# Optimization experiments

Measured on AMD Instinct MI355X. Metric: run time of the kernel, lower is better.

Reference implementation:

```python
import jax, jax.numpy as jnp
import numpy as np

B, S, DM, H = 4, 1024, 1024, 16
DK = DM // H  # 64, must equal embeddim=64

def _linear(x, W, b):
    # torch nn.Linear: y = x @ W.T + b, W is [out, in]
    return jnp.matmul(x, W.T) + b

def setup_inputs() -> dict:
    key = jax.random.key(0)
    ks = jax.random.split(key, 40)
    inp = {}
    inp["query"] = jax.random.normal(ks[0], (B, S, DM), jnp.float32)
    inp["key"] = jax.random.normal(ks[1], (B, S, DM), jnp.float32)
    inp["value"] = jax.random.normal(ks[2], (B, S, DM), jnp.float32)
    inp["mask"] = jnp.ones((B, S, S), jnp.int32)
    def mk(i, dout, din):
        W = jax.random.normal(ks[i], (dout, din), jnp.float32) / np.sqrt(din).astype(np.float32)
        b = jax.random.normal(ks[i + 20], (dout,), jnp.float32) * 0.01
        return W, b
    # the 4 d_model x d_model projection linears (q, k, v, out)
    inp["Wq"], inp["bq"] = mk(3, DM, DM)
    inp["Wk"], inp["bk"] = mk(4, DM, DM)
    inp["Wv"], inp["bv"] = mk(5, DM, DM)
    inp["Wo"], inp["bo"] = mk(6, DM, DM)
    # the 64x64 refinement linears
    inp["Wkl"], inp["bkl"] = mk(7, DK, DK)   # key_linear
    inp["Wql"], inp["bql"] = mk(8, DK, DK)   # query_linear
    inp["Wq2"], inp["bq2"] = mk(9, DK, DK)   # query2_linear
    inp["Wvl"], inp["bvl"] = mk(10, DK, DK)  # value_linear
    inp["Wel"], inp["bel"] = mk(11, DK, DK)  # embed_linear
    return inp

def reference(query, key, value, mask,
              Wq, bq, Wk, bk, Wv, bv, Wo, bo,
              Wkl, bkl, Wql, bql, Wq2, bq2, Wvl, bvl, Wel, bel):
    b, s, dm = query.shape
    # project and split heads: [b, h, s, d_k]
    def split(x):
        return x.reshape(b, s, H, DK).transpose(0, 2, 1, 3)
    q = split(_linear(query, Wq, bq))
    k = split(_linear(key, Wk, bk))
    v = split(_linear(value, Wv, bv))
    # per-head 64x64 refinements with relu
    key_refine = jax.nn.relu(_linear(k, Wkl, bkl))
    q1 = jax.nn.relu(_linear(q, Wql, bql))
    q1 = jax.nn.relu(_linear(q1, Wel, bel))
    q2 = jax.nn.relu(_linear(q, Wq2, bq2))
    v_refine = jax.nn.relu(_linear(v, Wvl, bvl))
    # two attention-like matmuls (no 1/sqrt(d_k) scaling in original)
    qv = jnp.einsum("bhqd,bhkd->bhqk", q2, v_refine)
    kq = jnp.einsum("bhqd,bhkd->bhqk", q1, key_refine)
    m = mask[:, None, :, :]  # mask.unsqueeze(1)
    kq = jnp.where(m == 0, jnp.float32(-1e9), kq)
    attn = jax.nn.softmax(kq, axis=-1)
    # elementwise combine, then matmul against raw projected key (not value!)
    out = jnp.einsum("bhqk,bhkd->bhqd", attn * qv, k)
    out = out.transpose(0, 2, 1, 3).reshape(b, s, dm)
    return _linear(out, Wo, bo)
```

## Files before the change

kernel.cpp:

```cpp
#include <hip/hip_runtime.h>
#include <hip/hip_bf16.h>

#define B_  4
#define S_  1024
#define DM_ 1024
#define H_  16
#define DK_ 64

typedef unsigned short u16;
typedef __attribute__((ext_vector_type(8))) short bf16x8;
typedef __attribute__((ext_vector_type(4))) float f32x4;

__device__ __forceinline__ float bf2f(u16 u) {
    union { unsigned int i; float f; } c;
    c.i = ((unsigned int)u) << 16;
    return c.f;
}
__device__ __forceinline__ u16 f2bf(float f) {
    union { float f; unsigned int i; } c;
    c.f = f;
    unsigned int x = c.i;
    unsigned int lsb = (x >> 16) & 1u;
    x += 0x7fffu + lsb;
    return (u16)(x >> 16);
}
__device__ __forceinline__ u16 f2bf_fast(float f) {
    __hip_bfloat16 h = __float2bfloat16(f);
    return *reinterpret_cast<u16*>(&h);
}

__device__ __forceinline__ void async_ld16(const u16* g, u16* l) {
    __builtin_amdgcn_global_load_lds(
        (const __attribute__((address_space(1))) unsigned int*)(const void*)g,
        (__attribute__((address_space(3))) unsigned int*)(void*)l, 16, 0, 0);
}

__global__ void detect_kernel(const u16* __restrict__ q, int* __restrict__ flag) {
    int lane = threadIdx.x & 63;
    int cnt = 0;
#pragma unroll
    for (int i = 0; i < 4; ++i) {
        u16 u = q[2 * (lane * 4 + i)];
        int e = (u >> 7) & 0xFF;
        cnt += (e >= 100 && e <= 140) ? 1 : 0;
    }
#pragma unroll
    for (int off = 1; off < 64; off <<= 1) cnt += __shfl_xor(cnt, off, 64);
    if (lane == 0) *flag = (cnt < 128) ? 1 : 0;
}

#define NSEG 12
struct CvtArgs {
    const void* src[NSEG];
    void*       dst[NSEG];
    unsigned    off[NSEG + 1];
};

__global__ __launch_bounds__(256) void prep_kernel(
    CvtArgs a, unsigned total, const int* __restrict__ flag,
    const int* __restrict__ mask, int* __restrict__ tflags)
{
    const int tid = threadIdx.x;
    if (blockIdx.x < 512) {
        const int bx = blockIdx.x;
        const int kt = bx & 15, b = (bx >> 4) & 3, z = bx >> 6;
        int ok = 1;
#pragma unroll
        for (int i = tid; i < 128 * 16; i += 256) {
            int row = z * 128 + (i >> 4), seg = i & 15;
            int4 m = *(const int4*)&mask[((size_t)b * S_ + row) * S_ + kt * 64 + seg * 4];
            ok &= (m.x != 0) & (m.y != 0) & (m.z != 0) & (m.w != 0);
        }
        if (!ok) atomicOr(&tflags[b * 16 + kt], 1);
        return;
    }
    if (!*flag) return;
    unsigned v = (blockIdx.x - 512) * 256 + tid;
    if (v >= total) return;
    int s = 0;
    while (s < NSEG - 1 && v >= a.off[s + 1]) ++s;
    unsigned local = v - a.off[s];
    u16* dp = (u16*)a.dst[s] + (size_t)local * 8;
    const float* sp = (const float*)a.src[s] + (size_t)local * 8;
    float4 x = *(const float4*)sp, y = *(const float4*)(sp + 4);
    u16 t[8] = {f2bf(x.x), f2bf(x.y), f2bf(x.z), f2bf(x.w),
                f2bf(y.x), f2bf(y.y), f2bf(y.z), f2bf(y.w)};
    *(uint4*)dp = *(uint4*)t;
}

__global__ __launch_bounds__(256) void transpose_kernel(
    const u16* __restrict__ kp, u16* __restrict__ kpt)
{
    __shared__ u16 T[64][65];
    const int s0 = blockIdx.x * 64, h = blockIdx.y, b = blockIdx.z;
    const int tid = threadIdx.x;
    const size_t base = (size_t)b * S_ * DM_ + (size_t)h * DK_;
    for (int c = tid; c < 512; c += 256) {
        int row = c >> 3, cc = (c & 7) * 8;
        union { uint4 v; u16 u[8]; } x;
        x.v = *(const uint4*)&kp[base + (size_t)(s0 + row) * DM_ + cc];
#pragma unroll
        for (int j = 0; j < 8; ++j) T[row][cc + j] = x.u[j];
    }
    __syncthreads();
    const size_t baseT = (size_t)(b * H_ + h) * DK_ * S_;
    for (int c = tid; c < 512; c += 256) {
        int d = c >> 3, ss = (c & 7) * 8;
        u16 t[8];
#pragma unroll
        for (int j = 0; j < 8; ++j) t[j] = T[ss + j][d];
        *(uint4*)&kpt[baseT + (size_t)d * S_ + s0 + ss] = *(uint4*)t;
    }
}

struct QKVArgs {
    const u16* A0[3]; const u16* A1[3];
    const u16* W0[3]; const u16* W1[3];
    const void* bias[3];
    const u16* R10[3]; const u16* R11[3];
    const void* rb1[3];
    const u16* R20; const u16* R21; const void* rb2;
    const u16* R30; const u16* R31; const void* rb3;
    u16 *Kp, *q1b, *q2r, *krb, *vrb;
};

__global__ __launch_bounds__(256, 3) void qkv_fused_kernel(
    QKVArgs a, const int* __restrict__ flag)
{
    __shared__ __align__(16) u16 smem[16384];
    u16 (*As)[64] = (u16(*)[64])smem;
    u16 (*Ws)[64] = (u16(*)[64])(smem + 8192);

    const int z = blockIdx.z;
    const int f = *flag;
    const u16* __restrict__ A = f ? a.A1[z] : a.A0[z];
    const u16* __restrict__ W = f ? a.W1[z] : a.W0[z];
    const void* biasp = a.bias[z];

    const int m0   = blockIdx.y * 128;
    const int n0   = blockIdx.x * 128;
    const int tid  = threadIdx.x;
    const int w    = tid >> 6;
    const int lane = tid & 63;
    const int l16  = lane & 15;
    const int quad = lane >> 4;
    const int wr   = (w >> 1) * 64;
    const int wc   = (w & 1) * 64;

    const int srow = lane >> 3;
    const int sgrp = (lane & 7) ^ srow;

    f32x4 acc[4][4];
#pragma unroll
    for (int rt = 0; rt < 4; ++rt)
#pragma unroll
        for (int ct = 0; ct < 4; ++ct) acc[rt][ct] = (f32x4){0.f, 0.f, 0.f, 0.f};

    for (int k0 = 0; k0 < DM_; k0 += 64) {
#pragma unroll
        for (int s = 0; s < 4; ++s) {
            int seg = w * 4 + s;
            async_ld16(&A[(size_t)(m0 + seg * 8 + srow) * DM_ + k0 + sgrp * 8],
                       &As[seg * 8][0]);
            async_ld16(&W[(size_t)(n0 + seg * 8 + srow) * DM_ + k0 + sgrp * 8],
                       &Ws[seg * 8][0]);
        }
        __syncthreads();
#pragma unroll
        for (int kk = 0; kk < 2; ++kk) {
            const int p = (kk * 4 + quad) ^ (l16 & 7);
            bf16x8 av[4], bv[4];
#pragma unroll
            for (int rt = 0; rt < 4; ++rt)
                av[rt] = *(const bf16x8*)&As[wr + rt * 16 + l16][p * 8];
#pragma unroll
            for (int ct = 0; ct < 4; ++ct)
                bv[ct] = *(const bf16x8*)&Ws[wc + ct * 16 + l16][p * 8];
#pragma unroll
            for (int rt = 0; rt < 4; ++rt)
#pragma unroll
                for (int ct = 0; ct < 4; ++ct)
                    acc[rt][ct] = __builtin_amdgcn_mfma_f32_16x16x32_bf16(
                        av[rt], bv[ct], acc[rt][ct], 0, 0, 0);
        }
        __syncthreads();
    }

    const int hcol = n0 + wc;
    u16 (*Es)[64] = (u16(*)[64])(smem + w * 4096);

#pragma unroll
    for (int ct = 0; ct < 4; ++ct) {
        int col = hcol + ct * 16 + l16;
        float bv = f ? ((const float*)biasp)[col] : bf2f(((const u16*)biasp)[col]);
#pragma unroll
        for (int rt = 0; rt < 4; ++rt)
#pragma unroll
            for (int r = 0; r < 4; ++r) {
                int ml = rt * 16 + quad * 4 + r;
                int cl = ct * 16 + l16;
                u16 bb = f2bf(acc[rt][ct][r] + bv);
                if (z == 1) a.Kp[(size_t)(m0 + wr + ml) * DM_ + col] = bb;
                Es[ml][((((cl >> 3) ^ (ml & 7)) << 3) | (cl & 7))] = bb;
            }
    }

    bf16x8 af[4][2];
#pragma unroll
    for (int rt = 0; rt < 4; ++rt)
#pragma unroll
        for (int kk = 0; kk < 2; ++kk)
            af[rt][kk] = *(const bf16x8*)
                &Es[rt * 16 + l16][(((kk * 4 + quad) ^ (l16 & 7)) << 3)];

    const u16* R1 = f ? a.R11[z] : a.R10[z];
    bf16x8 wb[2][4];
#pragma unroll
    for (int kk = 0; kk < 2; ++kk)
#pragma unroll
        for (int ct = 0; ct < 4; ++ct)
            wb[kk][ct] = *(const bf16x8*)
                &R1[(size_t)(ct * 16 + l16) * 64 + kk * 32 + quad * 8];

    f32x4 r1[4][4];
#pragma unroll
    for (int rt = 0; rt < 4; ++rt)
#pragma unroll
        for (int ct = 0; ct < 4; ++ct) r1[rt][ct] = (f32x4){0.f, 0.f, 0.f, 0.f};
#pragma unroll
    for (int kk = 0; kk < 2; ++kk)
#pragma unroll
        for (int rt = 0; rt < 4; ++rt)
#pragma unroll
            for (int ct = 0; ct < 4; ++ct)
                r1[rt][ct] = __builtin_amdgcn_mfma_f32_16x16x32_bf16(
                    af[rt][kk], wb[kk][ct], r1[rt][ct], 0, 0, 0);

    if (z != 0) {
        const void* rb = a.rb1[z];
        u16* out = (z == 1) ? a.krb : a.vrb;
#pragma unroll
        for (int ct = 0; ct < 4; ++ct) {
            int cl = ct * 16 + l16;
            float bv = f ? ((const float*)rb)[cl] : bf2f(((const u16*)rb)[cl]);
#pragma unroll
            for (int rt = 0; rt < 4; ++rt)
#pragma unroll
                for (int r = 0; r < 4; ++r) {
                    float v = r1[rt][ct][r] + bv;
                    v = v > 0.f ? v : 0.f;
                    out[(size_t)(m0 + wr + rt * 16 + quad * 4 + r) * DM_ + hcol + cl]
                        = f2bf(v);
                }
        }
    } else {
        {
            const void* rb = a.rb1[0];
#pragma unroll
            for (int ct = 0; ct < 4; ++ct) {
                int cl = ct * 16 + l16;
                float bv = f ? ((const float*)rb)[cl] : bf2f(((const u16*)rb)[cl]);
#pragma unroll
                for (int rt = 0; rt < 4; ++rt)
#pragma unroll
                    for (int r = 0; r < 4; ++r) {
                        float v = r1[rt][ct][r] + bv;
                        v = v > 0.f ? v : 0.f;
                        int ml = rt * 16 + quad * 4 + r;
                        Es[ml][((((cl >> 3) ^ (ml & 7)) << 3) | (cl & 7))] = f2bf(v);
                    }
            }
        }
        {
            const u16* R3 = f ? a.R31 : a.R30;
#pragma unroll
            for (int kk = 0; kk < 2; ++kk)
#pragma unroll
                for (int ct = 0; ct < 4; ++ct)
                    wb[kk][ct] = *(const bf16x8*)
                        &R3[(size_t)(ct * 16 + l16) * 64 + kk * 32 + quad * 8];
            f32x4 r3[4][4];
#pragma unroll
            for (int rt = 0; rt < 4; ++rt)
#pragma unroll
                for (int ct = 0; ct < 4; ++ct) r3[rt][ct] = (f32x4){0.f, 0.f, 0.f, 0.f};
#pragma unroll
            for (int kk = 0; kk < 2; ++kk)
#pragma unroll
                for (int rt = 0; rt < 4; ++rt)
#pragma unroll
                    for (int ct = 0; ct < 4; ++ct)
                        r3[rt][ct] = __builtin_amdgcn_mfma_f32_16x16x32_bf16(
                            af[rt][kk], wb[kk][ct], r3[rt][ct], 0, 0, 0);
            const void* rb = a.rb3;
#pragma unroll
            for (int ct = 0; ct < 4; ++ct) {
                int cl = ct * 16 + l16;
                float bv = f ? ((const float*)rb)[cl] : bf2f(((const u16*)rb)[cl]);
#pragma unroll
                for (int rt = 0; rt < 4; ++rt)
#pragma unroll
                    for (int r = 0; r < 4; ++r) {
                        float v = r3[rt][ct][r] + bv;
                        v = v > 0.f ? v : 0.f;
                        a.q2r[(size_t)(m0 + wr + rt * 16 + quad * 4 + r) * DM_
                              + hcol + cl] = f2bf(v);
                    }
            }
        }
        {
#pragma unroll
            for (int rt = 0; rt < 4; ++rt)
#pragma unroll
                for (int kk = 0; kk < 2; ++kk)
                    af[rt][kk] = *(const bf16x8*)
                        &Es[rt * 16 + l16][(((kk * 4 + quad) ^ (l16 & 7)) << 3)];
            const u16* R2 = f ? a.R21 : a.R20;
#pragma unroll
            for (int kk = 0; kk < 2; ++kk)
#pragma unroll
                for (int ct = 0; ct < 4; ++ct)
                    wb[kk][ct] = *(const bf16x8*)
                        &R2[(size_t)(ct * 16 + l16) * 64 + kk * 32 + quad * 8];
            f32x4 r2[4][4];
#pragma unroll
            for (int rt = 0; rt < 4; ++rt)
#pragma unroll
                for (int ct = 0; ct < 4; ++ct) r2[rt][ct] = (f32x4){0.f, 0.f, 0.f, 0.f};
#pragma unroll
            for (int kk = 0; kk < 2; ++kk)
#pragma unroll
                for (int rt = 0; rt < 4; ++rt)
#pragma unroll
                    for (int ct = 0; ct < 4; ++ct)
                        r2[rt][ct] = __builtin_amdgcn_mfma_f32_16x16x32_bf16(
                            af[rt][kk], wb[kk][ct], r2[rt][ct], 0, 0, 0);
            const void* rb = a.rb2;
#pragma unroll
            for (int ct = 0; ct < 4; ++ct) {
                int cl = ct * 16 + l16;
                float bv = f ? ((const float*)rb)[cl] : bf2f(((const u16*)rb)[cl]);
#pragma unroll
                for (int rt = 0; rt < 4; ++rt)
#pragma unroll
                    for (int r = 0; r < 4; ++r) {
                        float v = r2[rt][ct][r] + bv;
                        v = v > 0.f ? v : 0.f;
                        a.q1b[(size_t)(m0 + wr + rt * 16 + quad * 4 + r) * DM_
                              + hcol + cl] = f2bf(v);
                    }
            }
        }
    }
}

__global__ __launch_bounds__(256, 3) void gemm_async_kernel(
    const u16* __restrict__ Ain, const u16* __restrict__ W0,
    const u16* __restrict__ W1, const void* __restrict__ biasp,
    void* __restrict__ Cp, const int* __restrict__ flag)
{
    __shared__ __align__(16) u16 As[128][64];
    __shared__ __align__(16) u16 Ws[128][64];

    const int f = *flag;
    const u16* __restrict__ W = f ? W1 : W0;

    const int m0   = blockIdx.y * 128;
    const int n0   = blockIdx.x * 128;
    const int tid  = threadIdx.x;
    const int w    = tid >> 6;
    const int lane = tid & 63;
    const int l16  = lane & 15;
    const int quad = lane >> 4;
    const int wr   = (w >> 1) * 64;
    const int wc   = (w & 1) * 64;

    const int srow = lane >> 3;
    const int sgrp = (lane & 7) ^ srow;

    f32x4 acc[4][4];
#pragma unroll
    for (int rt = 0; rt < 4; ++rt)
#pragma unroll
        for (int ct = 0; ct < 4; ++ct) acc[rt][ct] = (f32x4){0.f, 0.f, 0.f, 0.f};

    for (int k0 = 0; k0 < DM_; k0 += 64) {
#pragma unroll
        for (int s = 0; s < 4; ++s) {
            int seg = w * 4 + s;
            async_ld16(&Ain[(size_t)(m0 + seg * 8 + srow) * DM_ + k0 + sgrp * 8],
                       &As[seg * 8][0]);
            async_ld16(&W[(size_t)(n0 + seg * 8 + srow) * DM_ + k0 + sgrp * 8],
                       &Ws[seg * 8][0]);
        }
        __syncthreads();
#pragma unroll
        for (int kk = 0; kk < 2; ++kk) {
            const int p = (kk * 4 + quad) ^ (l16 & 7);
            bf16x8 av[4], bv[4];
#pragma unroll
            for (int rt = 0; rt < 4; ++rt)
                av[rt] = *(const bf16x8*)&As[wr + rt * 16 + l16][p * 8];
#pragma unroll
            for (int ct = 0; ct < 4; ++ct)
                bv[ct] = *(const bf16x8*)&Ws[wc + ct * 16 + l16][p * 8];
#pragma unroll
            for (int rt = 0; rt < 4; ++rt)
#pragma unroll
                for (int ct = 0; ct < 4; ++ct)
                    acc[rt][ct] = __builtin_amdgcn_mfma_f32_16x16x32_bf16(
                        av[rt], bv[ct], acc[rt][ct], 0, 0, 0);
        }
        __syncthreads();
    }

#pragma unroll
    for (int ct = 0; ct < 4; ++ct) {
        int col = n0 + wc + ct * 16 + l16;
        float bv = f ? ((const float*)biasp)[col] : bf2f(((const u16*)biasp)[col]);
#pragma unroll
        for (int rt = 0; rt < 4; ++rt)
#pragma unroll
            for (int r = 0; r < 4; ++r) {
                int row = m0 + wr + rt * 16 + quad * 4 + r;
                float v = acc[rt][ct][r] + bv;
                size_t idx = (size_t)row * DM_ + col;
                if (f) ((float*)Cp)[idx] = v;
                else   ((u16*)Cp)[idx]   = f2bf(v);
            }
    }
}

__global__ __launch_bounds__(256, 2) void attn_kernel(
    const u16* __restrict__ q1, const u16* __restrict__ q2,
    const u16* __restrict__ kr, const u16* __restrict__ vr,
    const u16* __restrict__ kpt, const int* __restrict__ mask,
    const int* __restrict__ tflags, u16* __restrict__ om)
{
    __shared__ __align__(16) u16 krs[64][72];
    __shared__ __align__(16) u16 vrs[64][72];
    __shared__ __align__(16) u16 kts[64][72];
    __shared__ __align__(16) u16 pts[4][32][72];

    const int qt   = blockIdx.x;
    const int h    = blockIdx.y;
    const int b    = blockIdx.z;
    const int q0   = qt * 128;
    const int tid  = threadIdx.x;
    const int w    = tid >> 6;
    const int lane = tid & 63;
    const int l16  = lane & 15;
    const int quad = lane >> 4;

    const size_t base  = (size_t)b * S_ * DM_ + (size_t)h * DK_;
    const size_t baseT = (size_t)(b * H_ + h) * DK_ * S_;

    bf16x8 a1[2][2], a2[2][2];
#pragma unroll
    for (int rt = 0; rt < 2; ++rt) {
        const int qrow = q0 + w * 32 + rt * 16 + l16;
#pragma unroll
        for (int kk = 0; kk < 2; ++kk) {
            a1[rt][kk] = *(const bf16x8*)&q1[base + (size_t)qrow * DM_ + kk * 32 + quad * 8];
            a2[rt][kk] = *(const bf16x8*)&q2[base + (size_t)qrow * DM_ + kk * 32 + quad * 8];
        }
    }

    float m_run[2][4], l_run[2][4];
    f32x4 oacc[2][4];
#pragma unroll
    for (int rt = 0; rt < 2; ++rt)
#pragma unroll
        for (int r = 0; r < 4; ++r) { m_run[rt][r] = -1e30f; l_run[rt][r] = 0.f; }
#pragma unroll
    for (int rt = 0; rt < 2; ++rt)
#pragma unroll
        for (int ct = 0; ct < 4; ++ct) oacc[rt][ct] = (f32x4){0.f, 0.f, 0.f, 0.f};

    for (int kt = 0; kt < S_ / 64; ++kt) {
        const int k0 = kt * 64;
        __syncthreads();
        for (int c = tid; c < 512; c += 256) {
            int row = c >> 3, cc = (c & 7) * 8;
            *(uint4*)&krs[row][cc] = *(const uint4*)&kr[base + (size_t)(k0 + row) * DM_ + cc];
            *(uint4*)&vrs[row][cc] = *(const uint4*)&vr[base + (size_t)(k0 + row) * DM_ + cc];
            *(uint4*)&kts[row][cc] = *(const uint4*)&kpt[baseT + (size_t)row * S_ + k0 + cc];
        }
        __syncthreads();

        const int tf = tflags[b * 16 + kt];

        f32x4 s1[2][4], s2[2][4];
#pragma unroll
        for (int rt = 0; rt < 2; ++rt)
#pragma unroll
            for (int ct = 0; ct < 4; ++ct) {
                s1[rt][ct] = (f32x4){0.f, 0.f, 0.f, 0.f};
                s2[rt][ct] = (f32x4){0.f, 0.f, 0.f, 0.f};
            }
#pragma unroll
        for (int kk = 0; kk < 2; ++kk) {
            bf16x8 b1[4], b2[4];
#pragma unroll
            for (int ct = 0; ct < 4; ++ct) {
                b1[ct] = *(const bf16x8*)&krs[ct * 16 + l16][kk * 32 + quad * 8];
                b2[ct] = *(const bf16x8*)&vrs[ct * 16 + l16][kk * 32 + quad * 8];
            }
#pragma unroll
            for (int rt = 0; rt < 2; ++rt)
#pragma unroll
                for (int ct = 0; ct < 4; ++ct) {
                    s1[rt][ct] = __builtin_amdgcn_mfma_f32_16x16x32_bf16(
                        a1[rt][kk], b1[ct], s1[rt][ct], 0, 0, 0);
                    s2[rt][ct] = __builtin_amdgcn_mfma_f32_16x16x32_bf16(
                        a2[rt][kk], b2[ct], s2[rt][ct], 0, 0, 0);
                }
        }

        if (tf) {
#pragma unroll
            for (int rt = 0; rt < 2; ++rt)
#pragma unroll
                for (int ct = 0; ct < 4; ++ct)
#pragma unroll
                    for (int r = 0; r < 4; ++r) {
                        int qrow = q0 + w * 32 + rt * 16 + quad * 4 + r;
                        int kc   = k0 + ct * 16 + l16;
                        if (mask[((size_t)b * S_ + qrow) * S_ + kc] == 0)
                            s1[rt][ct][r] = -1e9f;
                    }
        }

        float tmax[2][4];
#pragma unroll
        for (int rt = 0; rt < 2; ++rt)
#pragma unroll
            for (int r = 0; r < 4; ++r) tmax[rt][r] = -1e30f;
#pragma unroll
        for (int rt = 0; rt < 2; ++rt)
#pragma unroll
            for (int ct = 0; ct < 4; ++ct)
#pragma unroll
                for (int r = 0; r < 4; ++r)
                    tmax[rt][r] = fmaxf(tmax[rt][r], s1[rt][ct][r]);
#pragma unroll
        for (int off = 1; off < 16; off <<= 1)
#pragma unroll
            for (int rt = 0; rt < 2; ++rt)
#pragma unroll
                for (int r = 0; r < 4; ++r)
                    tmax[rt][r] = fmaxf(tmax[rt][r], __shfl_xor(tmax[rt][r], off, 64));

        float alpha[2][4], newm[2][4];
#pragma unroll
        for (int rt = 0; rt < 2; ++rt)
#pragma unroll
            for (int r = 0; r < 4; ++r) {
                newm[rt][r]  = fmaxf(m_run[rt][r], tmax[rt][r]);
                alpha[rt][r] = __expf(m_run[rt][r] - newm[rt][r]);
                m_run[rt][r] = newm[rt][r];
            }

        float psum[2][4] = {};
#pragma unroll
        for (int rt = 0; rt < 2; ++rt)
#pragma unroll
            for (int ct = 0; ct < 4; ++ct)
#pragma unroll
                for (int r = 0; r < 4; ++r) {
                    float p = __expf(s1[rt][ct][r] - newm[rt][r]);
                    psum[rt][r] += p;
                    pts[w][rt * 16 + quad * 4 + r][ct * 16 + l16] =
                        f2bf_fast(p * s2[rt][ct][r]);
                }
#pragma unroll
        for (int off = 1; off < 16; off <<= 1)
#pragma unroll
            for (int rt = 0; rt < 2; ++rt)
#pragma unroll
                for (int r = 0; r < 4; ++r)
                    psum[rt][r] += __shfl_xor(psum[rt][r], off, 64);
#pragma unroll
        for (int rt = 0; rt < 2; ++rt)
#pragma unroll
            for (int r = 0; r < 4; ++r)
                l_run[rt][r] = l_run[rt][r] * alpha[rt][r] + psum[rt][r];
#pragma unroll
        for (int rt = 0; rt < 2; ++rt)
#pragma unroll
            for (int ct = 0; ct < 4; ++ct)
#pragma unroll
                for (int r = 0; r < 4; ++r) oacc[rt][ct][r] *= alpha[rt][r];

        {
            bf16x8 bb[2][4];
#pragma unroll
            for (int kk = 0; kk < 2; ++kk)
#pragma unroll
                for (int ct = 0; ct < 4; ++ct)
                    bb[kk][ct] = *(const bf16x8*)&kts[ct * 16 + l16][kk * 32 + quad * 8];
#pragma unroll
            for (int rt = 0; rt < 2; ++rt)
#pragma unroll
                for (int kk = 0; kk < 2; ++kk) {
                    bf16x8 a = *(const bf16x8*)&pts[w][rt * 16 + l16][kk * 32 + quad * 8];
#pragma unroll
                    for (int ct = 0; ct < 4; ++ct)
                        oacc[rt][ct] = __builtin_amdgcn_mfma_f32_16x16x32_bf16(
                            a, bb[kk][ct], oacc[rt][ct], 0, 0, 0);
                }
        }
    }

#pragma unroll
    for (int rt = 0; rt < 2; ++rt)
#pragma unroll
        for (int ct = 0; ct < 4; ++ct)
#pragma unroll
            for (int r = 0; r < 4; ++r) {
                int row = q0 + w * 32 + rt * 16 + quad * 4 + r;
                int col = ct * 16 + l16;
                float v = oacc[rt][ct][r] / l_run[rt][r];
                om[base + (size_t)row * DM_ + col] = f2bf_fast(v);
            }
}

extern "C" void kernel_launch(void* const* d_in, const int* in_sizes, int n_in,
                              void* d_out, int out_size, void* d_ws, size_t ws_size,
                              hipStream_t stream)
{
    const void* query = d_in[0];
    const void* key   = d_in[1];
    const void* value = d_in[2];
    const int*  mask  = (const int*)d_in[3];
    const void* Wq  = d_in[4];  const void* bq  = d_in[5];
    const void* Wk  = d_in[6];  const void* bk  = d_in[7];
    const void* Wv  = d_in[8];  const void* bv  = d_in[9];
    const void* Wo  = d_in[10]; const void* bo  = d_in[11];
    const void* Wkl = d_in[12]; const void* bkl = d_in[13];
    const void* Wql = d_in[14]; const void* bql = d_in[15];
    const void* Wq2 = d_in[16]; const void* bq2 = d_in[17];
    const void* Wvl = d_in[18]; const void* bvl = d_in[19];
    const void* Wel = d_in[20]; const void* bel = d_in[21];

    int* flag   = (int*)d_ws;
    int* tflags = (int*)d_ws + 4;
    u16* ws     = (u16*)((char*)d_ws + 512);
    const size_t BUF = (size_t)(B_ * S_) * DM_;
    u16* Kp  = ws + 0 * BUF;
    u16* krb = ws + 1 * BUF;
    u16* q1b = ws + 2 * BUF;
    u16* q2r = ws + 3 * BUF;
    u16* vrb = ws + 4 * BUF;
    u16* Om  = ws + 5 * BUF;
    u16* KpT = ws + 6 * BUF;
    u16* Qc  = ws + 7 * BUF;
    u16* Kc  = ws + 8 * BUF;
    u16* Vc  = ws + 9 * BUF;
    u16* Wbig = ws + 10 * BUF;
    u16* Wqc = Wbig + 0 * (size_t)(DM_ * DM_);
    u16* Wkc = Wbig + 1 * (size_t)(DM_ * DM_);
    u16* Wvc = Wbig + 2 * (size_t)(DM_ * DM_);
    u16* Woc = Wbig + 3 * (size_t)(DM_ * DM_);
    u16* Wsm = Wbig + 4 * (size_t)(DM_ * DM_);
    u16* Wklc = Wsm + 0 * (DK_ * DK_);
    u16* Wqlc = Wsm + 1 * (DK_ * DK_);
    u16* Welc = Wsm + 2 * (DK_ * DK_);
    u16* Wq2c = Wsm + 3 * (DK_ * DK_);
    u16* Wvlc = Wsm + 4 * (DK_ * DK_);

    const int M = B_ * S_;
    dim3 blk(256);

    detect_kernel<<<1, 64, 0, stream>>>((const u16*)query, flag);

    hipMemsetAsync(tflags, 0, 64 * sizeof(int), stream);
    CvtArgs ca;
    const unsigned VIN = (unsigned)(BUF / 8);
    const unsigned VWB = (unsigned)(DM_ * DM_ / 8);
    const unsigned VWS = (unsigned)(DK_ * DK_ / 8);
    const void* srcs[NSEG] = {query, key, value, Wq, Wk, Wv, Wo, Wkl, Wql, Wel, Wq2, Wvl};
    void* dsts[NSEG] = {Qc, Kc, Vc, Wqc, Wkc, Wvc, Woc, Wklc, Wqlc, Welc, Wq2c, Wvlc};
    unsigned vcn[NSEG] = {VIN, VIN, VIN, VWB, VWB, VWB, VWB, VWS, VWS, VWS, VWS, VWS};
    unsigned off = 0;
    for (int i = 0; i < NSEG; ++i) { ca.src[i] = srcs[i]; ca.dst[i] = dsts[i]; ca.off[i] = off; off += vcn[i]; }
    ca.off[NSEG] = off;
    prep_kernel<<<dim3(512 + (off + 255) / 256), blk, 0, stream>>>(ca, off, flag, mask, tflags);

    QKVArgs qa = {};
    qa.A0[0] = (const u16*)query; qa.A1[0] = Qc;
    qa.A0[1] = (const u16*)key;   qa.A1[1] = Kc;
    qa.A0[2] = (const u16*)value; qa.A1[2] = Vc;
    qa.W0[0] = (const u16*)Wq; qa.W1[0] = Wqc;
    qa.W0[1] = (const u16*)Wk; qa.W1[1] = Wkc;
    qa.W0[2] = (const u16*)Wv; qa.W1[2] = Wvc;
    qa.bias[0] = bq; qa.bias[1] = bk; qa.bias[2] = bv;
    qa.R10[0] = (const u16*)Wql; qa.R11[0] = Wqlc; qa.rb1[0] = bql;
    qa.R10[1] = (const u16*)Wkl; qa.R11[1] = Wklc; qa.rb1[1] = bkl;
    qa.R10[2] = (const u16*)Wvl; qa.R11[2] = Wvlc; qa.rb1[2] = bvl;
    qa.R20 = (const u16*)Wel; qa.R21 = Welc; qa.rb2 = bel;
    qa.R30 = (const u16*)Wq2; qa.R31 = Wq2c; qa.rb3 = bq2;
    qa.Kp = Kp; qa.q1b = q1b; qa.q2r = q2r; qa.krb = krb; qa.vrb = vrb;
    dim3 gBig(DM_ / 128, M / 128, 3);
    qkv_fused_kernel<<<gBig, blk, 0, stream>>>(qa, flag);

    dim3 gT(S_ / 64, H_, B_);
    transpose_kernel<<<gT, blk, 0, stream>>>(Kp, KpT);

    dim3 gA(S_ / 128, H_, B_);
    attn_kernel<<<gA, blk, 0, stream>>>(q1b, q2r, krb, vrb, KpT, mask, tflags, Om);

    dim3 gO(DM_ / 128, M / 128);
    gemm_async_kernel<<<gO, blk, 0, stream>>>(Om, (const u16*)Wo, Woc, bo, d_out, flag);
}
```

Baseline: 315.8 us.

## Double-buffer attention K/V tiles, swizzle blocks across XCDs, raise MFMA priority

The attention kernel now loads the next 64-key tile of key-refine, value-refine and transposed K into registers while the current tile is computed. It writes them into a second LDS buffer afterwards, so each iteration needs one barrier instead of two and global load latency is hidden. The 3D grid is flattened and remapped so consecutive blocks on the same XCD work on the same batch and head, aiming for better L2 reuse of K/V. s_setprio is raised around the MFMA sections. The cost is double the LDS for the K/V tiles, which may lower occupancy, plus extra registers for the prefetched data.

```diff
diff --git a/kernel.cpp b/kernel.cpp
--- a/kernel.cpp
+++ b/kernel.cpp
@@ -437,14 +437,17 @@
     const u16* __restrict__ kpt, const int* __restrict__ mask,
     const int* __restrict__ tflags, u16* __restrict__ om)
 {
-    __shared__ __align__(16) u16 krs[64][72];
-    __shared__ __align__(16) u16 vrs[64][72];
-    __shared__ __align__(16) u16 kts[64][72];
+    __shared__ __align__(16) u16 krs[2][64][72];
+    __shared__ __align__(16) u16 vrs[2][64][72];
+    __shared__ __align__(16) u16 kts[2][64][72];
     __shared__ __align__(16) u16 pts[4][32][72];
 
-    const int qt   = blockIdx.x;
-    const int h    = blockIdx.y;
-    const int b    = blockIdx.z;
+    const int bid  = blockIdx.x;
+    const int orig = (bid & 7) * 64 + (bid >> 3);
+    const int qt = orig & 7;
+    const int h  = (orig >> 3) & 15;
+    const int b  = orig >> 7;
+
     const int q0   = qt * 128;
     const int tid  = threadIdx.x;
     const int w    = tid >> 6;
@@ -455,6 +458,9 @@
     const size_t base  = (size_t)b * S_ * DM_ + (size_t)h * DK_;
     const size_t baseT = (size_t)(b * H_ + h) * DK_ * S_;
 
+    const int sr = tid >> 3;
+    const int sc = (tid & 7) * 8;
+
     bf16x8 a1[2][2], a2[2][2];
 #pragma unroll
     for (int rt = 0; rt < 2; ++rt) {
@@ -477,16 +483,37 @@
 #pragma unroll
         for (int ct = 0; ct < 4; ++ct) oacc[rt][ct] = (f32x4){0.f, 0.f, 0.f, 0.f};
 
+    {
+        uint4 ka = *(const uint4*)&kr[base + (size_t)(sr) * DM_ + sc];
+        uint4 kb = *(const uint4*)&kr[base + (size_t)(sr + 32) * DM_ + sc];
+        uint4 va = *(const uint4*)&vr[base + (size_t)(sr) * DM_ + sc];
+        uint4 vb = *(const uint4*)&vr[base + (size_t)(sr + 32) * DM_ + sc];
+        uint4 ta = *(const uint4*)&kpt[baseT + (size_t)sr * S_ + sc];
+        uint4 tb = *(const uint4*)&kpt[baseT + (size_t)(sr + 32) * S_ + sc];
+        *(uint4*)&krs[0][sr][sc]      = ka;
+        *(uint4*)&krs[0][sr + 32][sc] = kb;
+        *(uint4*)&vrs[0][sr][sc]      = va;
+        *(uint4*)&vrs[0][sr + 32][sc] = vb;
+        *(uint4*)&kts[0][sr][sc]      = ta;
+        *(uint4*)&kts[0][sr + 32][sc] = tb;
+    }
+    __syncthreads();
+
     for (int kt = 0; kt < S_ / 64; ++kt) {
-        const int k0 = kt * 64;
-        __syncthreads();
-        for (int c = tid; c < 512; c += 256) {
-            int row = c >> 3, cc = (c & 7) * 8;
-            *(uint4*)&krs[row][cc] = *(const uint4*)&kr[base + (size_t)(k0 + row) * DM_ + cc];
-            *(uint4*)&vrs[row][cc] = *(const uint4*)&vr[base + (size_t)(k0 + row) * DM_ + cc];
-            *(uint4*)&kts[row][cc] = *(const uint4*)&kpt[baseT + (size_t)row * S_ + k0 + cc];
-        }
-        __syncthreads();
+        const int cur = kt & 1;
+        const int k0  = kt * 64;
+        const bool pf = (kt + 1 < S_ / 64);
+
+        uint4 ka, kb, va, vb, ta, tb;
+        if (pf) {
+            const int kn = k0 + 64;
+            ka = *(const uint4*)&kr[base + (size_t)(kn + sr) * DM_ + sc];
+            kb = *(const uint4*)&kr[base + (size_t)(kn + sr + 32) * DM_ + sc];
+            va = *(const uint4*)&vr[base + (size_t)(kn + sr) * DM_ + sc];
+            vb = *(const uint4*)&vr[base + (size_t)(kn + sr + 32) * DM_ + sc];
+            ta = *(const uint4*)&kpt[baseT + (size_t)sr * S_ + kn + sc];
+            tb = *(const uint4*)&kpt[baseT + (size_t)(sr + 32) * S_ + kn + sc];
+        }
 
         const int tf = tflags[b * 16 + kt];
 
@@ -498,13 +525,14 @@
                 s1[rt][ct] = (f32x4){0.f, 0.f, 0.f, 0.f};
                 s2[rt][ct] = (f32x4){0.f, 0.f, 0.f, 0.f};
             }
+        __builtin_amdgcn_s_setprio(1);
 #pragma unroll
         for (int kk = 0; kk < 2; ++kk) {
             bf16x8 b1[4], b2[4];
 #pragma unroll
             for (int ct = 0; ct < 4; ++ct) {
-                b1[ct] = *(const bf16x8*)&krs[ct * 16 + l16][kk * 32 + quad * 8];
-                b2[ct] = *(const bf16x8*)&vrs[ct * 16 + l16][kk * 32 + quad * 8];
+                b1[ct] = *(const bf16x8*)&krs[cur][ct * 16 + l16][kk * 32 + quad * 8];
+                b2[ct] = *(const bf16x8*)&vrs[cur][ct * 16 + l16][kk * 32 + quad * 8];
             }
 #pragma unroll
             for (int rt = 0; rt < 2; ++rt)
@@ -516,6 +544,7 @@
                         a2[rt][kk], b2[ct], s2[rt][ct], 0, 0, 0);
                 }
         }
+        __builtin_amdgcn_s_setprio(0);
 
         if (tf) {
 #pragma unroll
@@ -593,12 +622,13 @@
                 for (int r = 0; r < 4; ++r) oacc[rt][ct][r] *= alpha[rt][r];
 
         {
+            __builtin_amdgcn_s_setprio(1);
             bf16x8 bb[2][4];
 #pragma unroll
             for (int kk = 0; kk < 2; ++kk)
 #pragma unroll
                 for (int ct = 0; ct < 4; ++ct)
-                    bb[kk][ct] = *(const bf16x8*)&kts[ct * 16 + l16][kk * 32 + quad * 8];
+                    bb[kk][ct] = *(const bf16x8*)&kts[cur][ct * 16 + l16][kk * 32 + quad * 8];
 #pragma unroll
             for (int rt = 0; rt < 2; ++rt)
 #pragma unroll
@@ -609,6 +639,18 @@
                         oacc[rt][ct] = __builtin_amdgcn_mfma_f32_16x16x32_bf16(
                             a, bb[kk][ct], oacc[rt][ct], 0, 0, 0);
                 }
+            __builtin_amdgcn_s_setprio(0);
+        }
+
+        if (pf) {
+            const int nxt = cur ^ 1;
+            *(uint4*)&krs[nxt][sr][sc]      = ka;
+            *(uint4*)&krs[nxt][sr + 32][sc] = kb;
+            *(uint4*)&vrs[nxt][sr][sc]      = va;
+            *(uint4*)&vrs[nxt][sr + 32][sc] = vb;
+            *(uint4*)&kts[nxt][sr][sc]      = ta;
+            *(uint4*)&kts[nxt][sr + 32][sc] = tb;
+            __syncthreads();
         }
     }
 
@@ -707,8 +749,7 @@
     dim3 gT(S_ / 64, H_, B_);
     transpose_kernel<<<gT, blk, 0, stream>>>(Kp, KpT);
 
-    dim3 gA(S_ / 128, H_, B_);
-    attn_kernel<<<gA, blk, 0, stream>>>(q1b, q2r, krb, vrb, KpT, mask, tflags, Om);
+    attn_kernel<<<dim3(512), blk, 0, stream>>>(q1b, q2r, krb, vrb, KpT, mask, tflags, Om);
 
     dim3 gO(DM_ / 128, M / 128);
     gemm_async_kernel<<<gO, blk, 0, stream>>>(Om, (const u16*)Wo, Woc, bo, d_out, flag);
```

Result: faster. 308.9 us (-2.2%).

## Load attention K/V tiles directly from global, remap blocks for L2 locality

Applied to the files above, without the earlier changes.

The attention kernel stops staging the key-refine, value-refine and transposed-key tiles in shared memory. Each lane now loads its MFMA B-operands straight from global memory, which removes two block barriers per key tile. Blocks are launched as a flat 1D grid, and the index is remapped so that the eight blocks on each XCD share the same (batch, head) K/V data. The change also raises launch bounds to 3 blocks per CU and wraps the MFMA sections in s_setprio. The cost is four redundant global/L2 reads of K/V per block, one per wave, instead of a single shared copy.

```diff
diff --git a/kernel.cpp b/kernel.cpp
--- a/kernel.cpp
+++ b/kernel.cpp
@@ -431,20 +431,20 @@
     }
 }
 
-__global__ __launch_bounds__(256, 2) void attn_kernel(
+__global__ __launch_bounds__(256, 3) void attn_kernel(
     const u16* __restrict__ q1, const u16* __restrict__ q2,
     const u16* __restrict__ kr, const u16* __restrict__ vr,
     const u16* __restrict__ kpt, const int* __restrict__ mask,
     const int* __restrict__ tflags, u16* __restrict__ om)
 {
-    __shared__ __align__(16) u16 krs[64][72];
-    __shared__ __align__(16) u16 vrs[64][72];
-    __shared__ __align__(16) u16 kts[64][72];
     __shared__ __align__(16) u16 pts[4][32][72];
 
-    const int qt   = blockIdx.x;
-    const int h    = blockIdx.y;
-    const int b    = blockIdx.z;
+    const int bid  = blockIdx.x;
+    const int orig = (bid & 7) * 64 + (bid >> 3);
+    const int qt = orig & 7;
+    const int h  = (orig >> 3) & 15;
+    const int b  = orig >> 7;
+
     const int q0   = qt * 128;
     const int tid  = threadIdx.x;
     const int w    = tid >> 6;
@@ -455,6 +455,10 @@
     const size_t base  = (size_t)b * S_ * DM_ + (size_t)h * DK_;
     const size_t baseT = (size_t)(b * H_ + h) * DK_ * S_;
 
+    const u16* __restrict__ krL = kr  + base  + (size_t)l16 * DM_ + quad * 8;
+    const u16* __restrict__ vrL = vr  + base  + (size_t)l16 * DM_ + quad * 8;
+    const u16* __restrict__ ktL = kpt + baseT + (size_t)l16 * S_  + quad * 8;
+
     bf16x8 a1[2][2], a2[2][2];
 #pragma unroll
     for (int rt = 0; rt < 2; ++rt) {
@@ -479,15 +483,6 @@
 
     for (int kt = 0; kt < S_ / 64; ++kt) {
         const int k0 = kt * 64;
-        __syncthreads();
-        for (int c = tid; c < 512; c += 256) {
-            int row = c >> 3, cc = (c & 7) * 8;
-            *(uint4*)&krs[row][cc] = *(const uint4*)&kr[base + (size_t)(k0 + row) * DM_ + cc];
-            *(uint4*)&vrs[row][cc] = *(const uint4*)&vr[base + (size_t)(k0 + row) * DM_ + cc];
-            *(uint4*)&kts[row][cc] = *(const uint4*)&kpt[baseT + (size_t)row * S_ + k0 + cc];
-        }
-        __syncthreads();
-
         const int tf = tflags[b * 16 + kt];
 
         f32x4 s1[2][4], s2[2][4];
@@ -498,13 +493,14 @@
                 s1[rt][ct] = (f32x4){0.f, 0.f, 0.f, 0.f};
                 s2[rt][ct] = (f32x4){0.f, 0.f, 0.f, 0.f};
             }
+        __builtin_amdgcn_s_setprio(1);
 #pragma unroll
         for (int kk = 0; kk < 2; ++kk) {
             bf16x8 b1[4], b2[4];
 #pragma unroll
             for (int ct = 0; ct < 4; ++ct) {
-                b1[ct] = *(const bf16x8*)&krs[ct * 16 + l16][kk * 32 + quad * 8];
-                b2[ct] = *(const bf16x8*)&vrs[ct * 16 + l16][kk * 32 + quad * 8];
+                b1[ct] = *(const bf16x8*)&krL[(size_t)(k0 + ct * 16) * DM_ + kk * 32];
+                b2[ct] = *(const bf16x8*)&vrL[(size_t)(k0 + ct * 16) * DM_ + kk * 32];
             }
 #pragma unroll
             for (int rt = 0; rt < 2; ++rt)
@@ -516,6 +512,7 @@
                         a2[rt][kk], b2[ct], s2[rt][ct], 0, 0, 0);
                 }
         }
+        __builtin_amdgcn_s_setprio(0);
 
         if (tf) {
 #pragma unroll
@@ -593,12 +590,13 @@
                 for (int r = 0; r < 4; ++r) oacc[rt][ct][r] *= alpha[rt][r];
 
         {
+            __builtin_amdgcn_s_setprio(1);
             bf16x8 bb[2][4];
 #pragma unroll
             for (int kk = 0; kk < 2; ++kk)
 #pragma unroll
                 for (int ct = 0; ct < 4; ++ct)
-                    bb[kk][ct] = *(const bf16x8*)&kts[ct * 16 + l16][kk * 32 + quad * 8];
+                    bb[kk][ct] = *(const bf16x8*)&ktL[(size_t)(ct * 16) * S_ + k0 + kk * 32];
 #pragma unroll
             for (int rt = 0; rt < 2; ++rt)
 #pragma unroll
@@ -609,6 +607,7 @@
                         oacc[rt][ct] = __builtin_amdgcn_mfma_f32_16x16x32_bf16(
                             a, bb[kk][ct], oacc[rt][ct], 0, 0, 0);
                 }
+            __builtin_amdgcn_s_setprio(0);
         }
     }
 
@@ -707,8 +706,7 @@
     dim3 gT(S_ / 64, H_, B_);
     transpose_kernel<<<gT, blk, 0, stream>>>(Kp, KpT);
 
-    dim3 gA(S_ / 128, H_, B_);
-    attn_kernel<<<gA, blk, 0, stream>>>(q1b, q2r, krb, vrb, KpT, mask, tflags, Om);
+    attn_kernel<<<dim3(512), blk, 0, stream>>>(q1b, q2r, krb, vrb, KpT, mask, tflags, Om);
 
     dim3 gO(DM_ / 128, M / 128);
     gemm_async_kernel<<<gO, blk, 0, stream>>>(Om, (const u16*)Wo, Woc, bo, d_out, flag);
```

After: 388.6 us. +23.0%, slower.
